# Optimization experiments

Measured on AMD Instinct MI355X. Metric: run time of the kernel, lower is better.

## Reference

```python
import jax, jax.numpy as jnp
import numpy as np

N, NF, DIM, H, DH, DEPTH, EDIM, NB = 256, 127, 128, 8, 64, 6, 3, 512
INNER = H * DH  # 512
SCALE = DH ** -0.5
EPS = 1e-5


def setup_inputs() -> dict:
    key = jax.random.key(0)
    ks = jax.random.split(key, 16)
    p = lambda k, shape: jax.random.normal(k, shape, jnp.float32) * 0.02
    return {
        "coordinates": jax.random.normal(ks[0], (N, 3), jnp.float32),
        "bonds": jax.random.randint(ks[1], (NB, 2), 0, N),
        "noise_level": jax.random.uniform(ks[2], (1,), jnp.float32),
        "atom_emb": p(ks[3], (N, NF)),
        "ln1_g": jnp.ones((DEPTH, DIM)), "ln1_b": jnp.zeros((DEPTH, DIM)),
        "Wq": p(ks[4], (DEPTH, DIM, INNER)), "bq": jnp.zeros((DEPTH, INNER)),
        "Wkv": p(ks[5], (DEPTH, DIM, 2 * INNER)), "bkv": jnp.zeros((DEPTH, 2 * INNER)),
        "We": p(ks[6], (DEPTH, EDIM, INNER)), "be": jnp.zeros((DEPTH, INNER)),
        "Wo": p(ks[7], (DEPTH, INNER, DIM)), "bo": jnp.zeros((DEPTH, DIM)),
        "Wg1": p(ks[8], (DEPTH, 3 * DIM)),
        "ln2_g": jnp.ones((DEPTH, DIM)), "ln2_b": jnp.zeros((DEPTH, DIM)),
        "W1": p(ks[9], (DEPTH, DIM, 4 * DIM)), "b1": jnp.zeros((DEPTH, 4 * DIM)),
        "W2": p(ks[10], (DEPTH, 4 * DIM, DIM)), "b2": jnp.zeros((DEPTH, DIM)),
        "Wg2": p(ks[11], (DEPTH, 3 * DIM)),
        "out_w": p(ks[12], (DIM, 1)), "out_b": jnp.zeros((1,)),
    }


def _layernorm(x, g, b):
    m = jnp.mean(x, axis=-1, keepdims=True)
    v = jnp.mean((x - m) ** 2, axis=-1, keepdims=True)
    return (x - m) * jax.lax.rsqrt(v + EPS) * g + b


def _gated_residual(x, res, Wg):
    # Linear(3*dim -> 1, no bias) then sigmoid; mask is all-True so no masking.
    gate = jax.nn.sigmoid(jnp.concatenate([x, res, x - res], axis=-1) @ Wg)[..., None]
    return x * gate + res * (1.0 - gate)


def _forward(coordinates, bonds, noise_level, atom_emb, ln1_g, ln1_b, Wq, bq,
             Wkv, bkv, We, be, Wo, bo, Wg1, ln2_g, ln2_b, W1, b1, W2, b2, Wg2,
             out_w, out_b):
    n = coordinates.shape[0]
    # nodes: [n, NF] atom embeddings (looked up at arange(n)) + noise column -> [n, DIM]
    noise_col = jnp.broadcast_to(noise_level.reshape(1, 1), (n, 1))
    nodes = jnp.concatenate([atom_emb, noise_col], axis=-1)
    # dense edge tensor [n, n, 3]: coordinate differences at bonded pairs, antisymmetric
    bi, bj = bonds[:, 0], bonds[:, 1]
    diff = coordinates[bi] - coordinates[bj]
    edges = jnp.zeros((n, n, EDIM), jnp.float32).at[bi, bj].set(diff).at[bj, bi].set(-diff)

    for l in range(DEPTH):
        # --- edge-biased multi-head attention (PreNorm) ---
        x = _layernorm(nodes, ln1_g[l], ln1_b[l])
        q = (x @ Wq[l] + bq[l]).reshape(n, H, DH).transpose(1, 0, 2)          # [h, i, d]
        kv = x @ Wkv[l] + bkv[l]
        k = kv[:, :INNER].reshape(n, H, DH).transpose(1, 0, 2)                # [h, j, d]
        v = kv[:, INNER:].reshape(n, H, DH).transpose(1, 0, 2)                # [h, j, d]
        e = (edges @ We[l] + be[l]).reshape(n, n, H, DH).transpose(2, 0, 1, 3)  # [h, i, j, d]
        k_ij = k[:, None, :, :] + e                                            # [h, i, j, d]
        v_ij = v[:, None, :, :] + e
        sim = jnp.einsum('hid,hijd->hij', q, k_ij) * SCALE
        attn = jax.nn.softmax(sim, axis=-1)  # mask is all ones -> no-op
        out = jnp.einsum('hij,hijd->hid', attn, v_ij)                          # [h, i, d]
        out = out.transpose(1, 0, 2).reshape(n, INNER) @ Wo[l] + bo[l]         # [n, DIM]
        nodes = _gated_residual(out, nodes, Wg1[l])
        # --- feedforward (PreNorm) + gated residual ---
        y = _layernorm(nodes, ln2_g[l], ln2_b[l])
        y = jax.nn.gelu(y @ W1[l] + b1[l], approximate=False) @ W2[l] + b2[l]
        nodes = _gated_residual(y, nodes, Wg2[l])

    energy = nodes @ out_w + out_b  # [n, 1]
    return energy[None, :, :]       # [1, n, 1]


def reference(coordinates, bonds, noise_level, atom_emb, ln1_g, ln1_b, Wq, bq,
              Wkv, bkv, We, be, Wo, bo, Wg1, ln2_g, ln2_b, W1, b1, W2, b2, Wg2,
              out_w, out_b):
    return _forward(coordinates, bonds, noise_level, atom_emb, ln1_g, ln1_b,
                    Wq, bq, Wkv, bkv, We, be, Wo, bo, Wg1, ln2_g, ln2_b,
                    W1, b1, W2, b2, Wg2, out_w, out_b)
```

## Files before the change

kernel.cpp:

```cpp
#include <hip/hip_runtime.h>

#define NN     256
#define NF     127
#define DIM    128
#define NH     8
#define DH     64
#define INNER  512
#define DEPTH  6
#define NB     512
#define ATTN_SCALE 0.125f
#define LN_EPS 1e-5f

__device__ __forceinline__ float wred_sum(float v){
#pragma unroll
  for(int o=32;o;o>>=1) v += __shfl_xor(v,o);
  return v;
}
__device__ __forceinline__ float wred_max(float v){
#pragma unroll
  for(int o=32;o;o>>=1) v = fmaxf(v,__shfl_xor(v,o));
  return v;
}
__device__ __forceinline__ float block_sum(float v, float* sred, int t){
  v = wred_sum(v);
  __syncthreads();
  if((t&63)==0) sred[t>>6]=v;
  __syncthreads();
  float s = 0.f;
#pragma unroll
  for(int w=0; w<8; w++) s += sred[w];
  return s;
}

__device__ __forceinline__ void dev_ln(const float* in, float* out,
                                       const float* g, const float* b,
                                       float* sred, int t){
  float v = (t<DIM)? in[t] : 0.f;
  float m = block_sum(v,sred,t) * (1.f/DIM);
  float d = (t<DIM)? (v-m) : 0.f;
  float var = block_sum(d*d,sred,t) * (1.f/DIM);
  float rs = rsqrtf(var + LN_EPS);
  if(t<DIM) out[t] = d*rs*g[t] + b[t];
  __syncthreads();
}

__device__ __forceinline__ void dev_qkv4(const float* xs, int i,
    const float* Wq, const float* bq, const float* Wkv, const float* bkv,
    const float* be, float* qg, float* kT, float* vg, float* redS, int t){
  {
    const int cg4 = (t&127)*4, rq = t>>7;
    float4 acc = make_float4(0.f,0.f,0.f,0.f);
#pragma unroll
    for(int f=rq*32; f<rq*32+32; f++){
      float x = xs[f];
      float4 w = *(const float4*)(Wq + f*INNER + cg4);
      acc.x=fmaf(x,w.x,acc.x); acc.y=fmaf(x,w.y,acc.y);
      acc.z=fmaf(x,w.z,acc.z); acc.w=fmaf(x,w.w,acc.w);
    }
    *(float4*)(redS + rq*INNER + cg4) = acc;
  }
  __syncthreads();
  qg[i*INNER+t] = bq[t] + redS[t] + redS[INNER+t] + redS[2*INNER+t] + redS[3*INNER+t];
  __syncthreads();
  {
    const int cg4 = (t&255)*4, rh = t>>8;
    float4 acc = make_float4(0.f,0.f,0.f,0.f);
#pragma unroll 8
    for(int f=rh*64; f<rh*64+64; f++){
      float x = xs[f];
      float4 w = *(const float4*)(Wkv + f*(2*INNER) + cg4);
      acc.x=fmaf(x,w.x,acc.x); acc.y=fmaf(x,w.y,acc.y);
      acc.z=fmaf(x,w.z,acc.z); acc.w=fmaf(x,w.w,acc.w);
    }
    *(float4*)(redS + rh*(2*INNER) + cg4) = acc;
  }
  __syncthreads();
#pragma unroll
  for(int cc=0; cc<2; cc++){
    int c = t + cc*512;
    float s = redS[c] + redS[2*INNER+c] + bkv[c];
    if(c < INNER) kT[c*NN+i]          = s + be[c];
    else          vg[i*INNER+c-INNER] = s + be[c-INNER];
  }
  __syncthreads();
}

__global__ __launch_bounds__(512) void k_qkv0(const float* atom_emb, const float* noise,
    float* nodes,
    const float* ln1_g, const float* ln1_b,
    const float* Wq, const float* bq, const float* Wkv, const float* bkv, const float* be,
    float* qg, float* kT, float* vg){
  __shared__ float nd[DIM], xs[DIM], sred[8], redS[2048];
  int t = threadIdx.x, i = blockIdx.x;
  if(t<DIM){
    float v = (t<NF)? atom_emb[i*NF+t] : noise[0];
    nd[t] = v;
    nodes[i*DIM+t] = v;
  }
  __syncthreads();
  dev_ln(nd, xs, ln1_g, ln1_b, sred, t);
  dev_qkv4(xs, i, Wq, bq, Wkv, bkv, be, qg, kT, vg, redS, t);
}

__global__ __launch_bounds__(512) void k_layer(
    float* nodes, const float* qg, const float* kT, const float* vg,
    float* qg_n, float* kT_n, float* vg_n,
    const int* bonds, const float* coords,
    const float* We,
    const float* Wo, const float* bo, const float* Wg1,
    const float* ln2_g, const float* ln2_b,
    const float* W1, const float* b1, const float* W2, const float* b2,
    const float* Wg2,
    const float* ln1_g_n, const float* ln1_b_n,
    const float* Wq_n, const float* bq_n, const float* Wkv_n, const float* bkv_n,
    const float* be_n, int has_next)
{
  __shared__ float nd[DIM], xs[DIM], qs[INNER], ao[INNER], o128[DIM];
  __shared__ float eL[NN*3], aW[NH*NN], redS[2048], sred[8], qWe[NH*3];
  const int t = threadIdx.x, i = blockIdx.x;

  if(t<DIM) nd[t] = nodes[i*DIM+t];
  qs[t] = qg[i*INNER+t];
  eL[t] = 0.f;
  if(t<NN) eL[512+t] = 0.f;
  __syncthreads();

  {
    int bi = bonds[2*t], bj = bonds[2*t+1];
    if(bi==i || bj==i){
      float dx = coords[3*bi+0] - coords[3*bj+0];
      float dy = coords[3*bi+1] - coords[3*bj+1];
      float dz = coords[3*bi+2] - coords[3*bj+2];
      if(bi==i){ eL[bj*3+0]=dx;  eL[bj*3+1]=dy;  eL[bj*3+2]=dz;  }
      if(bj==i){ eL[bi*3+0]=-dx; eL[bi*3+1]=-dy; eL[bi*3+2]=-dz; }
    }
  }
  __syncthreads();

  if(t < NH*3){
    int h = t/3, c = t%3;
    float acc = 0.f;
    for(int d=0; d<DH; d++) acc = fmaf(qs[h*DH+d], We[c*INNER + h*DH + d], acc);
    qWe[t] = acc;
  }
  __syncthreads();

  {
    const int h = t>>6, l = t&63, j0 = 4*l;
    const float* kTh = kT + (h*DH)*NN;
    float s0=0.f,s1=0.f,s2=0.f,s3=0.f;
#pragma unroll 8
    for(int o=0; o<DH; o++){
      float qv = qs[h*DH+o];
      float4 kk = *(const float4*)(kTh + o*NN + j0);
      s0=fmaf(qv,kk.x,s0); s1=fmaf(qv,kk.y,s1); s2=fmaf(qv,kk.z,s2); s3=fmaf(qv,kk.w,s3);
    }
    float w0=qWe[h*3+0], w1=qWe[h*3+1], w2=qWe[h*3+2];
    s0 += w0*eL[(j0+0)*3+0] + w1*eL[(j0+0)*3+1] + w2*eL[(j0+0)*3+2];
    s1 += w0*eL[(j0+1)*3+0] + w1*eL[(j0+1)*3+1] + w2*eL[(j0+1)*3+2];
    s2 += w0*eL[(j0+2)*3+0] + w1*eL[(j0+2)*3+1] + w2*eL[(j0+2)*3+2];
    s3 += w0*eL[(j0+3)*3+0] + w1*eL[(j0+3)*3+1] + w2*eL[(j0+3)*3+2];
    s0*=ATTN_SCALE; s1*=ATTN_SCALE; s2*=ATTN_SCALE; s3*=ATTN_SCALE;
    float mx = wred_max(fmaxf(fmaxf(s0,s1),fmaxf(s2,s3)));
    float p0=expf(s0-mx), p1=expf(s1-mx), p2=expf(s2-mx), p3=expf(s3-mx);
    float inv = 1.f / wred_sum(p0+p1+p2+p3);
    float a0=p0*inv, a1=p1*inv, a2=p2*inv, a3=p3*inv;
    float* aw = aW + h*NN;
    *(float4*)(aw + j0) = make_float4(a0,a1,a2,a3);
    float c0 = a0*eL[(j0+0)*3+0]+a1*eL[(j0+1)*3+0]+a2*eL[(j0+2)*3+0]+a3*eL[(j0+3)*3+0];
    float c1 = a0*eL[(j0+0)*3+1]+a1*eL[(j0+1)*3+1]+a2*eL[(j0+2)*3+1]+a3*eL[(j0+3)*3+1];
    float c2 = a0*eL[(j0+0)*3+2]+a1*eL[(j0+1)*3+2]+a2*eL[(j0+2)*3+2]+a3*eL[(j0+3)*3+2];
    c0 = wred_sum(c0); c1 = wred_sum(c1); c2 = wred_sum(c2);
    __builtin_amdgcn_wave_barrier();
    const int dq = (l&15)*4, jg = l>>4;
    const float* vb = vg + h*DH + dq;
    float4 acc = make_float4(0.f,0.f,0.f,0.f);
#pragma unroll 8
    for(int jj=0; jj<64; jj++){
      int j = jg*64 + jj;
      float a = aw[j];
      float4 vv = *(const float4*)(vb + j*INNER);
      acc.x=fmaf(a,vv.x,acc.x); acc.y=fmaf(a,vv.y,acc.y);
      acc.z=fmaf(a,vv.z,acc.z); acc.w=fmaf(a,vv.w,acc.w);
    }
#pragma unroll
    for(int o=16;o<64;o<<=1){
      acc.x += __shfl_xor(acc.x,o); acc.y += __shfl_xor(acc.y,o);
      acc.z += __shfl_xor(acc.z,o); acc.w += __shfl_xor(acc.w,o);
    }
    if(l<16){
      float4 we0 = *(const float4*)(We + 0*INNER + h*DH + dq);
      float4 we1 = *(const float4*)(We + 1*INNER + h*DH + dq);
      float4 we2 = *(const float4*)(We + 2*INNER + h*DH + dq);
      float4 o;
      o.x = acc.x + c0*we0.x + c1*we1.x + c2*we2.x;
      o.y = acc.y + c0*we0.y + c1*we1.y + c2*we2.y;
      o.z = acc.z + c0*we0.z + c1*we1.z + c2*we2.z;
      o.w = acc.w + c0*we0.w + c1*we1.w + c2*we2.w;
      *(float4*)(ao + h*DH + dq) = o;
    }
  }
  __syncthreads();

  {
    const int cg4 = (t&31)*4, rg = t>>5;
    float4 acc = make_float4(0.f,0.f,0.f,0.f);
#pragma unroll
    for(int r=rg*32; r<rg*32+32; r++){
      float a = ao[r];
      float4 w = *(const float4*)(Wo + r*DIM + cg4);
      acc.x=fmaf(a,w.x,acc.x); acc.y=fmaf(a,w.y,acc.y);
      acc.z=fmaf(a,w.z,acc.z); acc.w=fmaf(a,w.w,acc.w);
    }
    *(float4*)(redS + rg*DIM + cg4) = acc;
    __syncthreads();
    if(t<DIM){
      float s = bo[t];
#pragma unroll
      for(int g=0; g<16; g++) s += redS[g*DIM+t];
      o128[t] = s;
    }
    __syncthreads();
    float gv = 0.f;
    if(t<DIM){
      float o = o128[t], r = nd[t];
      gv = o*Wg1[t] + r*Wg1[DIM+t] + (o-r)*Wg1[2*DIM+t];
    }
    float gs = block_sum(gv, sred, t);
    float gate = 1.f/(1.f + expf(-gs));
    if(t<DIM) nd[t] = o128[t]*gate + nd[t]*(1.f-gate);
    __syncthreads();
  }

  dev_ln(nd, xs, ln2_g, ln2_b, sred, t);
  {
    const int cg4 = (t&127)*4, rq = t>>7;
    float4 acc = make_float4(0.f,0.f,0.f,0.f);
#pragma unroll
    for(int f=rq*32; f<rq*32+32; f++){
      float x = xs[f];
      float4 w = *(const float4*)(W1 + f*INNER + cg4);
      acc.x=fmaf(x,w.x,acc.x); acc.y=fmaf(x,w.y,acc.y);
      acc.z=fmaf(x,w.z,acc.z); acc.w=fmaf(x,w.w,acc.w);
    }
    *(float4*)(redS + rq*INNER + cg4) = acc;
  }
  __syncthreads();
  {
    float a = b1[t] + redS[t] + redS[INNER+t] + redS[2*INNER+t] + redS[3*INNER+t];
    qs[t] = 0.5f*a*(1.f + erff(a*0.70710678118654752440f));
  }
  __syncthreads();
  {
    const int cg4 = (t&31)*4, rg = t>>5;
    float4 acc = make_float4(0.f,0.f,0.f,0.f);
#pragma unroll
    for(int m=rg*32; m<rg*32+32; m++){
      float a = qs[m];
      float4 w = *(const float4*)(W2 + m*DIM + cg4);
      acc.x=fmaf(a,w.x,acc.x); acc.y=fmaf(a,w.y,acc.y);
      acc.z=fmaf(a,w.z,acc.z); acc.w=fmaf(a,w.w,acc.w);
    }
    *(float4*)(redS + rg*DIM + cg4) = acc;
    __syncthreads();
    if(t<DIM){
      float s = b2[t];
#pragma unroll
      for(int g=0; g<16; g++) s += redS[g*DIM+t];
      o128[t] = s;
    }
    __syncthreads();
    float gv = 0.f;
    if(t<DIM){
      float y = o128[t], r = nd[t];
      gv = y*Wg2[t] + r*Wg2[DIM+t] + (y-r)*Wg2[2*DIM+t];
    }
    float gs = block_sum(gv, sred, t);
    float gate = 1.f/(1.f + expf(-gs));
    if(t<DIM) nd[t] = o128[t]*gate + nd[t]*(1.f-gate);
    __syncthreads();
  }
  if(t<DIM) nodes[i*DIM+t] = nd[t];

  if(has_next){
    dev_ln(nd, xs, ln1_g_n, ln1_b_n, sred, t);
    dev_qkv4(xs, i, Wq_n, bq_n, Wkv_n, bkv_n, be_n, qg_n, kT_n, vg_n, redS, t);
  }
}

__global__ __launch_bounds__(64) void k_energy(const float* nodes, const float* out_w,
                                               const float* out_b, float* out){
  int i = blockIdx.x, l = threadIdx.x;
  float a = fmaf(nodes[i*DIM+l], out_w[l], nodes[i*DIM+64+l]*out_w[64+l]);
  a = wred_sum(a);
  if(l==0) out[i] = a + out_b[0];
}

extern "C" void kernel_launch(void* const* d_in, const int* in_sizes, int n_in,
                              void* d_out, int out_size, void* d_ws, size_t ws_size,
                              hipStream_t stream){
  const float* coords   = (const float*)d_in[0];
  const int*   bonds    = (const int*  )d_in[1];
  const float* noise    = (const float*)d_in[2];
  const float* atom_emb = (const float*)d_in[3];
  const float* ln1_g = (const float*)d_in[4];
  const float* ln1_b = (const float*)d_in[5];
  const float* Wq    = (const float*)d_in[6];
  const float* bq    = (const float*)d_in[7];
  const float* Wkv   = (const float*)d_in[8];
  const float* bkv   = (const float*)d_in[9];
  const float* We    = (const float*)d_in[10];
  const float* be    = (const float*)d_in[11];
  const float* Wo    = (const float*)d_in[12];
  const float* bo    = (const float*)d_in[13];
  const float* Wg1   = (const float*)d_in[14];
  const float* ln2_g = (const float*)d_in[15];
  const float* ln2_b = (const float*)d_in[16];
  const float* W1    = (const float*)d_in[17];
  const float* b1    = (const float*)d_in[18];
  const float* W2    = (const float*)d_in[19];
  const float* b2    = (const float*)d_in[20];
  const float* Wg2   = (const float*)d_in[21];
  const float* out_w = (const float*)d_in[22];
  const float* out_b = (const float*)d_in[23];

  float* ws = (float*)d_ws;
  float* nodes   = ws;
  float* qbuf[2] = { ws +  32768, ws + 163840 };
  float* kbuf[2] = { ws + 294912, ws + 425984 };
  float* vbuf[2] = { ws + 557056, ws + 688128 };

  k_qkv0<<<256, 512, 0, stream>>>(atom_emb, noise, nodes, ln1_g, ln1_b,
                                  Wq, bq, Wkv, bkv, be,
                                  qbuf[0], kbuf[0], vbuf[0]);
  for(int l=0; l<DEPTH; l++){
    int cur = l&1, nxt = cur^1;
    int has_next = (l < DEPTH-1);
    int ln = has_next ? l+1 : l;
    k_layer<<<256, 512, 0, stream>>>(
      nodes, qbuf[cur], kbuf[cur], vbuf[cur],
      qbuf[nxt], kbuf[nxt], vbuf[nxt],
      bonds, coords,
      We  + (size_t)l*3*INNER,
      Wo  + (size_t)l*INNER*DIM, bo + (size_t)l*DIM, Wg1 + (size_t)l*3*DIM,
      ln2_g + (size_t)l*DIM, ln2_b + (size_t)l*DIM,
      W1  + (size_t)l*DIM*4*DIM, b1 + (size_t)l*4*DIM,
      W2  + (size_t)l*4*DIM*DIM, b2 + (size_t)l*DIM, Wg2 + (size_t)l*3*DIM,
      ln1_g + (size_t)ln*DIM, ln1_b + (size_t)ln*DIM,
      Wq  + (size_t)ln*DIM*INNER, bq + (size_t)ln*INNER,
      Wkv + (size_t)ln*DIM*2*INNER, bkv + (size_t)ln*2*INNER,
      be  + (size_t)ln*INNER, has_next);
  }
  k_energy<<<256, 64, 0, stream>>>(nodes, out_w, out_b, (float*)d_out);
}
```

Baseline: 320.1 us.

## Store K/V in fp16 and widen per-thread matvec tiles to 8 columns

K and V activations between layers are now stored as half precision, which halves the global-memory traffic of the attention score and value passes; they are converted back to float on load. All weight matvecs (Wq, Wkv, Wo, W1, W2) now have each thread compute 8 output columns over a shorter row slice, which doubles the partial-sum buffer and lengthens the reduction. Launch bounds now request 2 blocks per CU. The fp16 storage of K/V adds rounding error relative to the fp32 reference.

```diff
diff --git a/kernel.cpp b/kernel.cpp
--- a/kernel.cpp
+++ b/kernel.cpp
@@ -1,4 +1,5 @@
 #include <hip/hip_runtime.h>
+#include <hip/hip_fp16.h>
 
 #define NN     256
 #define NF     127
@@ -11,6 +12,13 @@
 #define ATTN_SCALE 0.125f
 #define LN_EPS 1e-5f
 
+__device__ __forceinline__ float4 ldh4(const __half* p){
+  __half2 h0 = ((const __half2*)p)[0];
+  __half2 h1 = ((const __half2*)p)[1];
+  float2 a = __half22float2(h0), b = __half22float2(h1);
+  return make_float4(a.x, a.y, b.x, b.y);
+}
+
 __device__ __forceinline__ float wred_sum(float v){
 #pragma unroll
   for(int o=32;o;o>>=1) v += __shfl_xor(v,o);
@@ -44,53 +52,68 @@
   __syncthreads();
 }
 
-__device__ __forceinline__ void dev_qkv4(const float* xs, int i,
+__device__ __forceinline__ void dev_qkv8(const float* xs, int i,
     const float* Wq, const float* bq, const float* Wkv, const float* bkv,
-    const float* be, float* qg, float* kT, float* vg, float* redS, int t){
-  {
-    const int cg4 = (t&127)*4, rq = t>>7;
-    float4 acc = make_float4(0.f,0.f,0.f,0.f);
+    const float* be, float* qg, __half* kT, __half* vg, float* redS, int t){
+  {
+    const int cg8 = (t&63)*8, rg = t>>6;
+    float4 a0 = make_float4(0.f,0.f,0.f,0.f);
+    float4 a1 = make_float4(0.f,0.f,0.f,0.f);
+#pragma unroll
+    for(int f=rg*16; f<rg*16+16; f++){
+      float x = xs[f];
+      float4 w0 = *(const float4*)(Wq + f*INNER + cg8);
+      float4 w1 = *(const float4*)(Wq + f*INNER + cg8 + 4);
+      a0.x=fmaf(x,w0.x,a0.x); a0.y=fmaf(x,w0.y,a0.y);
+      a0.z=fmaf(x,w0.z,a0.z); a0.w=fmaf(x,w0.w,a0.w);
+      a1.x=fmaf(x,w1.x,a1.x); a1.y=fmaf(x,w1.y,a1.y);
+      a1.z=fmaf(x,w1.z,a1.z); a1.w=fmaf(x,w1.w,a1.w);
+    }
+    *(float4*)(redS + rg*INNER + cg8)     = a0;
+    *(float4*)(redS + rg*INNER + cg8 + 4) = a1;
+  }
+  __syncthreads();
+  {
+    float s = bq[t];
+#pragma unroll
+    for(int g=0; g<8; g++) s += redS[g*INNER + t];
+    qg[i*INNER+t] = s;
+  }
+  __syncthreads();
+  {
+    const int cg8 = (t&127)*8, rq = t>>7;
+    float4 a0 = make_float4(0.f,0.f,0.f,0.f);
+    float4 a1 = make_float4(0.f,0.f,0.f,0.f);
 #pragma unroll
     for(int f=rq*32; f<rq*32+32; f++){
       float x = xs[f];
-      float4 w = *(const float4*)(Wq + f*INNER + cg4);
-      acc.x=fmaf(x,w.x,acc.x); acc.y=fmaf(x,w.y,acc.y);
-      acc.z=fmaf(x,w.z,acc.z); acc.w=fmaf(x,w.w,acc.w);
-    }
-    *(float4*)(redS + rq*INNER + cg4) = acc;
-  }
-  __syncthreads();
-  qg[i*INNER+t] = bq[t] + redS[t] + redS[INNER+t] + redS[2*INNER+t] + redS[3*INNER+t];
-  __syncthreads();
-  {
-    const int cg4 = (t&255)*4, rh = t>>8;
-    float4 acc = make_float4(0.f,0.f,0.f,0.f);
-#pragma unroll 8
-    for(int f=rh*64; f<rh*64+64; f++){
-      float x = xs[f];
-      float4 w = *(const float4*)(Wkv + f*(2*INNER) + cg4);
-      acc.x=fmaf(x,w.x,acc.x); acc.y=fmaf(x,w.y,acc.y);
-      acc.z=fmaf(x,w.z,acc.z); acc.w=fmaf(x,w.w,acc.w);
-    }
-    *(float4*)(redS + rh*(2*INNER) + cg4) = acc;
+      float4 w0 = *(const float4*)(Wkv + f*(2*INNER) + cg8);
+      float4 w1 = *(const float4*)(Wkv + f*(2*INNER) + cg8 + 4);
+      a0.x=fmaf(x,w0.x,a0.x); a0.y=fmaf(x,w0.y,a0.y);
+      a0.z=fmaf(x,w0.z,a0.z); a0.w=fmaf(x,w0.w,a0.w);
+      a1.x=fmaf(x,w1.x,a1.x); a1.y=fmaf(x,w1.y,a1.y);
+      a1.z=fmaf(x,w1.z,a1.z); a1.w=fmaf(x,w1.w,a1.w);
+    }
+    *(float4*)(redS + rq*1024 + cg8)     = a0;
+    *(float4*)(redS + rq*1024 + cg8 + 4) = a1;
   }
   __syncthreads();
 #pragma unroll
   for(int cc=0; cc<2; cc++){
     int c = t + cc*512;
-    float s = redS[c] + redS[2*INNER+c] + bkv[c];
-    if(c < INNER) kT[c*NN+i]          = s + be[c];
-    else          vg[i*INNER+c-INNER] = s + be[c-INNER];
-  }
-  __syncthreads();
-}
-
-__global__ __launch_bounds__(512) void k_qkv0(const float* atom_emb, const float* noise,
+    float s = redS[c] + redS[1024+c] + redS[2048+c] + redS[3072+c] + bkv[c];
+    if(c < INNER) kT[c*NN+i]          = __float2half(s + be[c]);
+    else          vg[i*INNER+c-INNER] = __float2half(s + be[c-INNER]);
+  }
+  __syncthreads();
+}
+
+__global__ __launch_bounds__(512,2) void k_qkv0(const float* atom_emb, const float* noise,
     float* nodes,
     const float* ln1_g, const float* ln1_b,
     const float* Wq, const float* bq, const float* Wkv, const float* bkv, const float* be,
-    float* qg, float* kT, float* vg){
-  __shared__ float nd[DIM], xs[DIM], sred[8], redS[2048];
+    float* qg, __half* kT, __half* vg){
+  __shared__ float nd[DIM], xs[DIM], sred[8], redS[4096];
   int t = threadIdx.x, i = blockIdx.x;
   if(t<DIM){
     float v = (t<NF)? atom_emb[i*NF+t] : noise[0];
@@ -99,12 +122,12 @@
   }
   __syncthreads();
   dev_ln(nd, xs, ln1_g, ln1_b, sred, t);
-  dev_qkv4(xs, i, Wq, bq, Wkv, bkv, be, qg, kT, vg, redS, t);
-}
-
-__global__ __launch_bounds__(512) void k_layer(
-    float* nodes, const float* qg, const float* kT, const float* vg,
-    float* qg_n, float* kT_n, float* vg_n,
+  dev_qkv8(xs, i, Wq, bq, Wkv, bkv, be, qg, kT, vg, redS, t);
+}
+
+__global__ __launch_bounds__(512,2) void k_layer(
+    float* nodes, const float* qg, const __half* kT, const __half* vg,
+    float* qg_n, __half* kT_n, __half* vg_n,
     const int* bonds, const float* coords,
     const float* We,
     const float* Wo, const float* bo, const float* Wg1,
@@ -116,7 +139,7 @@
     const float* be_n, int has_next)
 {
   __shared__ float nd[DIM], xs[DIM], qs[INNER], ao[INNER], o128[DIM];
-  __shared__ float eL[NN*3], aW[NH*NN], redS[2048], sred[8], qWe[NH*3];
+  __shared__ float eL[NN*3], aW[NH*NN], redS[4096], sred[8], qWe[NH*3];
   const int t = threadIdx.x, i = blockIdx.x;
 
   if(t<DIM) nd[t] = nodes[i*DIM+t];
@@ -147,12 +170,12 @@
 
   {
     const int h = t>>6, l = t&63, j0 = 4*l;
-    const float* kTh = kT + (h*DH)*NN;
+    const __half* kTh = kT + (h*DH)*NN;
     float s0=0.f,s1=0.f,s2=0.f,s3=0.f;
 #pragma unroll 8
     for(int o=0; o<DH; o++){
       float qv = qs[h*DH+o];
-      float4 kk = *(const float4*)(kTh + o*NN + j0);
+      float4 kk = ldh4(kTh + o*NN + j0);
       s0=fmaf(qv,kk.x,s0); s1=fmaf(qv,kk.y,s1); s2=fmaf(qv,kk.z,s2); s3=fmaf(qv,kk.w,s3);
     }
     float w0=qWe[h*3+0], w1=qWe[h*3+1], w2=qWe[h*3+2];
@@ -172,52 +195,71 @@
     float c2 = a0*eL[(j0+0)*3+2]+a1*eL[(j0+1)*3+2]+a2*eL[(j0+2)*3+2]+a3*eL[(j0+3)*3+2];
     c0 = wred_sum(c0); c1 = wred_sum(c1); c2 = wred_sum(c2);
     __builtin_amdgcn_wave_barrier();
-    const int dq = (l&15)*4, jg = l>>4;
-    const float* vb = vg + h*DH + dq;
-    float4 acc = make_float4(0.f,0.f,0.f,0.f);
+    const int dq = (l&7)*8, jg = l>>3;
+    const __half* vb = vg + h*DH + dq;
+    float4 accA = make_float4(0.f,0.f,0.f,0.f);
+    float4 accB = make_float4(0.f,0.f,0.f,0.f);
 #pragma unroll 8
-    for(int jj=0; jj<64; jj++){
-      int j = jg*64 + jj;
+    for(int jj=0; jj<32; jj++){
+      int j = jg*32 + jj;
       float a = aw[j];
-      float4 vv = *(const float4*)(vb + j*INNER);
-      acc.x=fmaf(a,vv.x,acc.x); acc.y=fmaf(a,vv.y,acc.y);
-      acc.z=fmaf(a,vv.z,acc.z); acc.w=fmaf(a,vv.w,acc.w);
-    }
-#pragma unroll
-    for(int o=16;o<64;o<<=1){
-      acc.x += __shfl_xor(acc.x,o); acc.y += __shfl_xor(acc.y,o);
-      acc.z += __shfl_xor(acc.z,o); acc.w += __shfl_xor(acc.w,o);
-    }
-    if(l<16){
-      float4 we0 = *(const float4*)(We + 0*INNER + h*DH + dq);
-      float4 we1 = *(const float4*)(We + 1*INNER + h*DH + dq);
-      float4 we2 = *(const float4*)(We + 2*INNER + h*DH + dq);
-      float4 o;
-      o.x = acc.x + c0*we0.x + c1*we1.x + c2*we2.x;
-      o.y = acc.y + c0*we0.y + c1*we1.y + c2*we2.y;
-      o.z = acc.z + c0*we0.z + c1*we1.z + c2*we2.z;
-      o.w = acc.w + c0*we0.w + c1*we1.w + c2*we2.w;
-      *(float4*)(ao + h*DH + dq) = o;
-    }
-  }
-  __syncthreads();
-
-  {
-    const int cg4 = (t&31)*4, rg = t>>5;
-    float4 acc = make_float4(0.f,0.f,0.f,0.f);
-#pragma unroll
-    for(int r=rg*32; r<rg*32+32; r++){
+      float4 v0 = ldh4(vb + j*INNER);
+      float4 v1 = ldh4(vb + j*INNER + 4);
+      accA.x=fmaf(a,v0.x,accA.x); accA.y=fmaf(a,v0.y,accA.y);
+      accA.z=fmaf(a,v0.z,accA.z); accA.w=fmaf(a,v0.w,accA.w);
+      accB.x=fmaf(a,v1.x,accB.x); accB.y=fmaf(a,v1.y,accB.y);
+      accB.z=fmaf(a,v1.z,accB.z); accB.w=fmaf(a,v1.w,accB.w);
+    }
+#pragma unroll
+    for(int o=8;o<64;o<<=1){
+      accA.x += __shfl_xor(accA.x,o); accA.y += __shfl_xor(accA.y,o);
+      accA.z += __shfl_xor(accA.z,o); accA.w += __shfl_xor(accA.w,o);
+      accB.x += __shfl_xor(accB.x,o); accB.y += __shfl_xor(accB.y,o);
+      accB.z += __shfl_xor(accB.z,o); accB.w += __shfl_xor(accB.w,o);
+    }
+    if(l<8){
+      float4 we00 = *(const float4*)(We + 0*INNER + h*DH + dq);
+      float4 we01 = *(const float4*)(We + 0*INNER + h*DH + dq + 4);
+      float4 we10 = *(const float4*)(We + 1*INNER + h*DH + dq);
+      float4 we11 = *(const float4*)(We + 1*INNER + h*DH + dq + 4);
+      float4 we20 = *(const float4*)(We + 2*INNER + h*DH + dq);
+      float4 we21 = *(const float4*)(We + 2*INNER + h*DH + dq + 4);
+      float4 oA, oB;
+      oA.x = accA.x + c0*we00.x + c1*we10.x + c2*we20.x;
+      oA.y = accA.y + c0*we00.y + c1*we10.y + c2*we20.y;
+      oA.z = accA.z + c0*we00.z + c1*we10.z + c2*we20.z;
+      oA.w = accA.w + c0*we00.w + c1*we10.w + c2*we20.w;
+      oB.x = accB.x + c0*we01.x + c1*we11.x + c2*we21.x;
+      oB.y = accB.y + c0*we01.y + c1*we11.y + c2*we21.y;
+      oB.z = accB.z + c0*we01.z + c1*we11.z + c2*we21.z;
+      oB.w = accB.w + c0*we01.w + c1*we11.w + c2*we21.w;
+      *(float4*)(ao + h*DH + dq)     = oA;
+      *(float4*)(ao + h*DH + dq + 4) = oB;
+    }
+  }
+  __syncthreads();
+
+  {
+    const int cg8 = (t&15)*8, rg = t>>4;
+    float4 a0 = make_float4(0.f,0.f,0.f,0.f);
+    float4 a1 = make_float4(0.f,0.f,0.f,0.f);
+#pragma unroll
+    for(int r=rg*16; r<rg*16+16; r++){
       float a = ao[r];
-      float4 w = *(const float4*)(Wo + r*DIM + cg4);
-      acc.x=fmaf(a,w.x,acc.x); acc.y=fmaf(a,w.y,acc.y);
-      acc.z=fmaf(a,w.z,acc.z); acc.w=fmaf(a,w.w,acc.w);
-    }
-    *(float4*)(redS + rg*DIM + cg4) = acc;
+      float4 w0 = *(const float4*)(Wo + r*DIM + cg8);
+      float4 w1 = *(const float4*)(Wo + r*DIM + cg8 + 4);
+      a0.x=fmaf(a,w0.x,a0.x); a0.y=fmaf(a,w0.y,a0.y);
+      a0.z=fmaf(a,w0.z,a0.z); a0.w=fmaf(a,w0.w,a0.w);
+      a1.x=fmaf(a,w1.x,a1.x); a1.y=fmaf(a,w1.y,a1.y);
+      a1.z=fmaf(a,w1.z,a1.z); a1.w=fmaf(a,w1.w,a1.w);
+    }
+    *(float4*)(redS + rg*DIM + cg8)     = a0;
+    *(float4*)(redS + rg*DIM + cg8 + 4) = a1;
     __syncthreads();
     if(t<DIM){
       float s = bo[t];
 #pragma unroll
-      for(int g=0; g<16; g++) s += redS[g*DIM+t];
+      for(int g=0; g<32; g++) s += redS[g*DIM+t];
       o128[t] = s;
     }
     __syncthreads();
@@ -234,39 +276,51 @@
 
   dev_ln(nd, xs, ln2_g, ln2_b, sred, t);
   {
-    const int cg4 = (t&127)*4, rq = t>>7;
-    float4 acc = make_float4(0.f,0.f,0.f,0.f);
-#pragma unroll
-    for(int f=rq*32; f<rq*32+32; f++){
+    const int cg8 = (t&63)*8, rg = t>>6;
+    float4 a0 = make_float4(0.f,0.f,0.f,0.f);
+    float4 a1 = make_float4(0.f,0.f,0.f,0.f);
+#pragma unroll
+    for(int f=rg*16; f<rg*16+16; f++){
       float x = xs[f];
-      float4 w = *(const float4*)(W1 + f*INNER + cg4);
-      acc.x=fmaf(x,w.x,acc.x); acc.y=fmaf(x,w.y,acc.y);
-      acc.z=fmaf(x,w.z,acc.z); acc.w=fmaf(x,w.w,acc.w);
-    }
-    *(float4*)(redS + rq*INNER + cg4) = acc;
-  }
-  __syncthreads();
-  {
-    float a = b1[t] + redS[t] + redS[INNER+t] + redS[2*INNER+t] + redS[3*INNER+t];
+      float4 w0 = *(const float4*)(W1 + f*INNER + cg8);
+      float4 w1 = *(const float4*)(W1 + f*INNER + cg8 + 4);
+      a0.x=fmaf(x,w0.x,a0.x); a0.y=fmaf(x,w0.y,a0.y);
+      a0.z=fmaf(x,w0.z,a0.z); a0.w=fmaf(x,w0.w,a0.w);
+      a1.x=fmaf(x,w1.x,a1.x); a1.y=fmaf(x,w1.y,a1.y);
+      a1.z=fmaf(x,w1.z,a1.z); a1.w=fmaf(x,w1.w,a1.w);
+    }
+    *(float4*)(redS + rg*INNER + cg8)     = a0;
+    *(float4*)(redS + rg*INNER + cg8 + 4) = a1;
+  }
+  __syncthreads();
+  {
+    float a = b1[t];
+#pragma unroll
+    for(int g=0; g<8; g++) a += redS[g*INNER + t];
     qs[t] = 0.5f*a*(1.f + erff(a*0.70710678118654752440f));
   }
   __syncthreads();
   {
-    const int cg4 = (t&31)*4, rg = t>>5;
-    float4 acc = make_float4(0.f,0.f,0.f,0.f);
-#pragma unroll
-    for(int m=rg*32; m<rg*32+32; m++){
+    const int cg8 = (t&15)*8, rg = t>>4;
+    float4 a0 = make_float4(0.f,0.f,0.f,0.f);
+    float4 a1 = make_float4(0.f,0.f,0.f,0.f);
+#pragma unroll
+    for(int m=rg*16; m<rg*16+16; m++){
       float a = qs[m];
-      float4 w = *(const float4*)(W2 + m*DIM + cg4);
-      acc.x=fmaf(a,w.x,acc.x); acc.y=fmaf(a,w.y,acc.y);
-      acc.z=fmaf(a,w.z,acc.z); acc.w=fmaf(a,w.w,acc.w);
-    }
-    *(float4*)(redS + rg*DIM + cg4) = acc;
+      float4 w0 = *(const float4*)(W2 + m*DIM + cg8);
+      float4 w1 = *(const float4*)(W2 + m*DIM + cg8 + 4);
+      a0.x=fmaf(a,w0.x,a0.x); a0.y=fmaf(a,w0.y,a0.y);
+      a0.z=fmaf(a,w0.z,a0.z); a0.w=fmaf(a,w0.w,a0.w);
+      a1.x=fmaf(a,w1.x,a1.x); a1.y=fmaf(a,w1.y,a1.y);
+      a1.z=fmaf(a,w1.z,a1.z); a1.w=fmaf(a,w1.w,a1.w);
+    }
+    *(float4*)(redS + rg*DIM + cg8)     = a0;
+    *(float4*)(redS + rg*DIM + cg8 + 4) = a1;
     __syncthreads();
     if(t<DIM){
       float s = b2[t];
 #pragma unroll
-      for(int g=0; g<16; g++) s += redS[g*DIM+t];
+      for(int g=0; g<32; g++) s += redS[g*DIM+t];
       o128[t] = s;
     }
     __syncthreads();
@@ -284,7 +338,7 @@
 
   if(has_next){
     dev_ln(nd, xs, ln1_g_n, ln1_b_n, sred, t);
-    dev_qkv4(xs, i, Wq_n, bq_n, Wkv_n, bkv_n, be_n, qg_n, kT_n, vg_n, redS, t);
+    dev_qkv8(xs, i, Wq_n, bq_n, Wkv_n, bkv_n, be_n, qg_n, kT_n, vg_n, redS, t);
   }
 }
 
@@ -324,11 +378,12 @@
   const float* out_w = (const float*)d_in[22];
   const float* out_b = (const float*)d_in[23];
 
-  float* ws = (float*)d_ws;
-  float* nodes   = ws;
-  float* qbuf[2] = { ws +  32768, ws + 163840 };
-  float* kbuf[2] = { ws + 294912, ws + 425984 };
-  float* vbuf[2] = { ws + 557056, ws + 688128 };
+  float* ws_f = (float*)d_ws;
+  float* nodes   = ws_f;
+  float* qbuf[2] = { ws_f + 32768, ws_f + 163840 };
+  __half* hb = (__half*)(ws_f + 294912);
+  __half* kbuf[2] = { hb,          hb + 131072 };
+  __half* vbuf[2] = { hb + 262144, hb + 393216 };
 
   k_qkv0<<<256, 512, 0, stream>>>(atom_emb, noise, nodes, ln1_g, ln1_b,
                                   Wq, bq, Wkv, bkv, be,
```

New measurement: 326.7 us. 2.1% more time.
